# Kernel tuning notes

Hardware: AMD Instinct MI355X
Metric: run time of the kernel (lower is better)

Reference implementation:

```python
import jax, jax.numpy as jnp
import numpy as np

H = 31  # hidden_size == input_size


def setup_inputs() -> dict:
    key = jax.random.key(0)
    ks = jax.random.split(key, 7)
    B, T = 2048, 512
    s = 1.0 / np.sqrt(H)
    return {
        "x": jax.random.normal(ks[0], (B, T, H), dtype=jnp.float32),
        "W_ih": jax.random.uniform(ks[1], (3 * H, H), minval=-s, maxval=s, dtype=jnp.float32),
        "W_hh": jax.random.uniform(ks[2], (3 * H, H), minval=-s, maxval=s, dtype=jnp.float32),
        "b_ih": jax.random.uniform(ks[3], (3 * H,), minval=-s, maxval=s, dtype=jnp.float32),
        "b_hh": jax.random.uniform(ks[4], (3 * H,), minval=-s, maxval=s, dtype=jnp.float32),
        "W_fc": jax.random.uniform(ks[5], (2, H), minval=-s, maxval=s, dtype=jnp.float32),
        "b_fc": jax.random.uniform(ks[6], (2,), minval=-s, maxval=s, dtype=jnp.float32),
    }


def _gru_seq(x, W_ih, W_hh, b_ih, b_hh):
    # x: [B, T, I]. Precompute input-side gates for all timesteps (one big GEMM).
    B = x.shape[0]
    xg = jnp.einsum("bti,gi->btg", x, W_ih) + b_ih          # [B, T, 3H]
    xg = jnp.swapaxes(xg, 0, 1)                              # [T, B, 3H]

    def step(h, xg_t):
        gh = h @ W_hh.T + b_hh                               # [B, 3H]
        ir, iz, inn = jnp.split(xg_t, 3, axis=-1)
        hr, hz, hn = jnp.split(gh, 3, axis=-1)
        r = jax.nn.sigmoid(ir + hr)
        z = jax.nn.sigmoid(iz + hz)
        n = jnp.tanh(inn + r * hn)
        h_new = (1.0 - z) * n + z * h
        return h_new, h_new

    h0 = jnp.zeros((B, H), dtype=x.dtype)
    _, out = jax.lax.scan(step, h0, xg)                      # out: [T, B, H]
    return jnp.swapaxes(out, 0, 1)                           # [B, T, H]


def reference(x, W_ih, W_hh, b_ih, b_hh, W_fc, b_fc):
    out = _gru_seq(x, W_ih, W_hh, b_ih, b_hh)                # [B, T, H]
    return out @ W_fc.T + b_fc                               # [B, T, 2]
```

## Files before the change

### kernel.cpp

```cpp
#include <hip/hip_runtime.h>


constexpr int BB = 2048, TT = 512, HH = 31;
constexpr int RR = 96;
constexpr size_t XG_BYTES = (size_t)BB * RR * TT * 2;
constexpr int WPAIRS = 93 * 16;
constexpr size_t WS_NEEDED = XG_BYTES + (size_t)WPAIRS * 4;
constexpr float LOG2E = 1.4426950408889634f;

#define MEMFENCE asm volatile("" ::: "memory")

typedef _Float16 hf2 __attribute__((ext_vector_type(2)));

__device__ __forceinline__ float dot2(int a, hf2 w, float acc) {
#if __has_builtin(__builtin_amdgcn_fdot2)
    return __builtin_amdgcn_fdot2(__builtin_bit_cast(hf2, a), w, acc, false);
#else
    hf2 x = __builtin_bit_cast(hf2, a);
    return acc + (float)x.x * (float)w.x + (float)x.y * (float)w.y;
#endif
}

__device__ __forceinline__ float fast_exp2(float x) {
#if __has_builtin(__builtin_amdgcn_exp2f)
    return __builtin_amdgcn_exp2f(x);
#else
    return exp2f(x);
#endif
}
__device__ __forceinline__ float fast_rcp(float x) {
#if __has_builtin(__builtin_amdgcn_rcpf)
    return __builtin_amdgcn_rcpf(x);
#else
    return __fdividef(1.f, x);
#endif
}

#if __has_builtin(__builtin_amdgcn_permlane32_swap)
__device__ __forceinline__ float xor32_swap(float v) {
    auto p = __builtin_amdgcn_permlane32_swap(
        __builtin_bit_cast(unsigned, v), __builtin_bit_cast(unsigned, v),
        false, false);
    return __builtin_bit_cast(float, (unsigned)p[0]) +
           __builtin_bit_cast(float, (unsigned)p[1]) - v;
}
#else
__device__ __forceinline__ float xor32_swap(float v) { return __shfl_xor(v, 32); }
#endif

__device__ __forceinline__ void bcast_h(float hv, int hs[16]) {
    const int pk = __builtin_bit_cast(int, __builtin_amdgcn_cvt_pkrtz(hv, hv));
#if __has_builtin(__builtin_amdgcn_update_dpp)
    const int nb = __builtin_amdgcn_update_dpp(0, pk, 0xB1, 0xF, 0xF, true);
#else
    const int nb = __shfl_xor(pk, 1);
#endif
    const int pr = __builtin_amdgcn_perm(nb, pk, 0x05040100);
#pragma unroll
    for (int m = 0; m < 16; ++m)
        hs[m] = __builtin_amdgcn_readlane(pr, 2 * m);
}

__global__ void pack_wih_kernel(const float* __restrict__ W_ih, int* __restrict__ wpk) {
    int q = blockIdx.x * blockDim.x + threadIdx.x;
    if (q >= WPAIRS) return;
    int row = q >> 4, p = q & 15;
    const float s = (row < 62) ? LOG2E : 2.f * LOG2E;
    float lo = W_ih[row * HH + 2 * p] * s;
    float hi = (2 * p + 1 < HH) ? W_ih[row * HH + 2 * p + 1] * s : 0.f;
    hf2 w; w.x = (_Float16)lo; w.y = (_Float16)hi;
    wpk[q] = __builtin_bit_cast(int, w);
}

__global__ __launch_bounds__(128, 2) void xg_gemm_kernel(
    const float* __restrict__ x, const int* __restrict__ wpk,
    const float* __restrict__ b_ih, _Float16* __restrict__ xg)
{
    const int tid = threadIdx.x;
    const int b   = blockIdx.x;
    const int t0  = tid * 4;
    const float* xb = x + ((size_t)b * TT + t0) * HH;

    hf2 xp[4][16];
#pragma unroll
    for (int j = 0; j < 4; ++j)
#pragma unroll
        for (int p = 0; p < 16; ++p) {
            float lo = xb[j * HH + 2 * p];
            float hi = (2 * p + 1 < HH) ? xb[j * HH + 2 * p + 1] : 0.f;
            xp[j][p].x = (_Float16)lo; xp[j][p].y = (_Float16)hi;
        }

    _Float16* xgb = xg + (size_t)b * RR * TT + t0;
    for (int row = 0; row < 93; ++row) {
        const float bi = b_ih[row] * ((row < 62) ? LOG2E : 2.f * LOG2E);
        float a0 = bi, a1 = bi, a2 = bi, a3 = bi;
        const int* wr = wpk + row * 16;
#pragma unroll
        for (int p = 0; p < 16; ++p) {
            const int w = wr[p];
            a0 = dot2(w, xp[0][p], a0);
            a1 = dot2(w, xp[1][p], a1);
            a2 = dot2(w, xp[2][p], a2);
            a3 = dot2(w, xp[3][p], a3);
        }
        hf2 lo2; lo2.x = (_Float16)a0; lo2.y = (_Float16)a1;
        hf2 hi2; hi2.x = (_Float16)a2; hi2.y = (_Float16)a3;
        *reinterpret_cast<int2*>(xgb + (size_t)row * TT) =
            make_int2(__builtin_bit_cast(int, lo2), __builtin_bit_cast(int, hi2));
    }
    for (int row = 93; row < 96; ++row)
        *reinterpret_cast<int2*>(xgb + (size_t)row * TT) = make_int2(0, 0);
}

__global__ __launch_bounds__(256, 2) void gru_rec_kernel(
    const _Float16* __restrict__ xg, const float* __restrict__ W_hh,
    const float* __restrict__ b_hh, const float* __restrict__ W_fc,
    const float* __restrict__ b_fc, float* __restrict__ out)
{
    const int tid = threadIdx.x, wv = tid >> 6, lane = tid & 63;
    const int li = lane & 31, half = lane >> 5;
    const int b  = blockIdx.x * 4 + wv;
    const bool u = (li < HH);

    const float sA = u ? LOG2E : 1.f;
    const float sN = 2.f * LOG2E;
    const float* pA = u ? W_hh + (size_t)(half * HH + li) * HH
                        : W_fc + (size_t)half * HH;
    const float* pN = W_hh + (size_t)(2 * HH + (u ? li : 0)) * HH;
    const float bA0 = (u ? b_hh[half * HH + li] : b_fc[half]) * sA;
    const float bN0 = u ? b_hh[2 * HH + li] * sN : 0.f;

    hf2 wA[16], wN[16];
#pragma unroll
    for (int p = 0; p < 16; ++p) {
        const float alo = pA[2 * p];
        const float ahi = (2 * p + 1 < HH) ? pA[2 * p + 1] : 0.f;
        wA[p].x = (_Float16)(alo * sA); wA[p].y = (_Float16)(ahi * sA);
        const float nlo = u ? pN[2 * p] : 0.f;
        const float nhi = (u && 2 * p + 1 < HH) ? pN[2 * p + 1] : 0.f;
        wN[p].x = (_Float16)(nlo * sN); wN[p].y = (_Float16)(nhi * sN);
    }

    const int rowA = u ? half * HH + li : 93 + half;
    const int rowN = u ? 2 * HH + li : 95;
    const _Float16* gA = xg + ((size_t)b * RR + rowA) * TT;
    const _Float16* gN = xg + ((size_t)b * RR + rowN) * TT;
    float* outb = out + (size_t)b * TT * 2;

    float hval = 0.f;
    int hs[16];
    bcast_h(0.f, hs);

    int4 bufA = *(const int4*)gA;
    int4 bufN = *(const int4*)gN;

    for (int tb = 0; tb < TT / 8; ++tb) {
        int4 nxtA = bufA, nxtN = bufN;
        if (tb + 1 < TT / 8) {
            nxtA = *(const int4*)(gA + (size_t)(tb + 1) * 8);
            nxtN = *(const int4*)(gN + (size_t)(tb + 1) * 8);
        }
#pragma unroll
        for (int s = 0; s < 8; ++s) {
            const int t = tb * 8 + s;
            const float xa = (float)(((const _Float16*)&bufA)[s]);
            const float xn = (float)(((const _Float16*)&bufN)[s]);

            float a0 = bA0 + xa, a1 = 0.f, n0 = bN0, n1 = 0.f;
#pragma unroll
            for (int m = 0; m < 16; m += 2) {
                a0 = dot2(hs[m],     wA[m],     a0);
                a1 = dot2(hs[m + 1], wA[m + 1], a1);
                n0 = dot2(hs[m],     wN[m],     n0);
                n1 = dot2(hs[m + 1], wN[m + 1], n1);
            }
            const float accA = a0 + a1;
            const float accN = n0 + n1;
            const float asw = xor32_swap(accA);

            if (li == 31 && t > 0) outb[(size_t)(t - 1) * 2 + half] = accA;

            const float g  = fast_rcp(1.f + fast_exp2(-accA));
            const float go = fast_rcp(1.f + fast_exp2(-asw));
            const float r = half ? go : g;
            const float z = half ? g : go;
            const float en = fast_exp2(fmaf(-r, accN, -xn));
            const float nn = fmaf(2.f, fast_rcp(1.f + en), -1.f);
            const float hnew = nn + z * (hval - nn);
            hval = u ? hnew : 0.f;
            bcast_h(hval, hs);
        }
        bufA = nxtA; bufN = nxtN;
    }

    {
        float a0 = bA0, a1 = 0.f;
#pragma unroll
        for (int m = 0; m < 16; m += 2) {
            a0 = dot2(hs[m],     wA[m],     a0);
            a1 = dot2(hs[m + 1], wA[m + 1], a1);
        }
        if (li == 31) outb[(size_t)(TT - 1) * 2 + half] = a0 + a1;
    }
}

__global__ __launch_bounds__(64, 1) void gru_pair_kernel(
    const float* __restrict__ x, const float* __restrict__ W_ih,
    const float* __restrict__ W_hh, const float* __restrict__ b_ih,
    const float* __restrict__ b_hh, const float* __restrict__ W_fc,
    const float* __restrict__ b_fc, float* __restrict__ out)
{
    __shared__ _Float16 hbuf[2][32];
    __shared__ _Float16 xbuf[2][2][32];

    const int lane = threadIdx.x & 63;
    const int li   = lane & 31;
    const int half = lane >> 5;
    const int b    = blockIdx.x * 2 + half;
    const bool unit = (li < HH);

    const float* ph0 = unit ? W_hh + (size_t)li * HH            : W_fc;
    const float* ph1 = unit ? W_hh + (size_t)(HH + li) * HH     : W_fc + HH;
    const float* ph2 = unit ? W_hh + (size_t)(2 * HH + li) * HH : nullptr;
    const float* px0 = unit ? W_ih + (size_t)li * HH            : nullptr;
    const float* px1 = unit ? W_ih + (size_t)(HH + li) * HH     : nullptr;
    const float* px2 = unit ? W_ih + (size_t)(2 * HH + li) * HH : nullptr;

    hf2 wh0[16], wh1[16], wh2[16], wx0[16], wx1[16], wx2[16];
#pragma unroll
    for (int m = 0; m < 16; ++m) {
        auto pk = [&](const float* p) -> hf2 {
            hf2 r;
            r.x = p ? (_Float16)p[2 * m] : (_Float16)0.f;
            r.y = (p && (2 * m + 1) < HH) ? (_Float16)p[2 * m + 1] : (_Float16)0.f;
            return r;
        };
        wh0[m] = pk(ph0); wh1[m] = pk(ph1); wh2[m] = pk(ph2);
        wx0[m] = pk(px0); wx1[m] = pk(px1); wx2[m] = pk(px2);
    }

    float arH0, azH0, anH0, anX0;
    if (unit) {
        arH0 = b_ih[li] + b_hh[li];
        azH0 = b_ih[HH + li] + b_hh[HH + li];
        anH0 = b_hh[2 * HH + li];
        anX0 = b_ih[2 * HH + li];
    } else {
        arH0 = b_fc[0]; azH0 = b_fc[1]; anH0 = 0.f; anX0 = 0.f;
    }

    const float* xb   = x + (size_t)b * TT * HH;
    float*       outb = out + (size_t)b * TT * 2;

    hbuf[half][li]    = (_Float16)0.f;
    xbuf[0][half][li] = unit ? (_Float16)xb[li]      : (_Float16)0.f;
    xbuf[1][half][li] = unit ? (_Float16)xb[HH + li] : (_Float16)0.f;
    MEMFENCE;
    float xpre = unit ? xb[(size_t)2 * HH + li] : 0.f;
    float hval = 0.f;

    const int4* HP  = (const int4*)(&hbuf[half][0]);
    const int4* XB0 = (const int4*)(&xbuf[0][half][0]);
    const int4* XB1 = (const int4*)(&xbuf[1][half][0]);

    int4 xq0 = XB0[0], xq1 = XB0[1], xq2 = XB0[2], xq3 = XB0[3];

#pragma unroll 2
    for (int t = 0; t < TT; ++t) {
        int4 hq0 = HP[0], hq1 = HP[1], hq2 = HP[2], hq3 = HP[3];

        float arH = arH0, azH = azH0, anH = anH0;
        float arX = 0.f, azX = 0.f, anX = anX0;
#define STEPM(m, hp, xp) \
        arH = dot2(hp, wh0[m], arH); azH = dot2(hp, wh1[m], azH); \
        anH = dot2(hp, wh2[m], anH); arX = dot2(xp, wx0[m], arX); \
        azX = dot2(xp, wx1[m], azX); anX = dot2(xp, wx2[m], anX);
        STEPM(0,  hq0.x, xq0.x) STEPM(1,  hq0.y, xq0.y)
        STEPM(2,  hq0.z, xq0.z) STEPM(3,  hq0.w, xq0.w)
        STEPM(4,  hq1.x, xq1.x) STEPM(5,  hq1.y, xq1.y)
        STEPM(6,  hq1.z, xq1.z) STEPM(7,  hq1.w, xq1.w)
        STEPM(8,  hq2.x, xq2.x) STEPM(9,  hq2.y, xq2.y)
        STEPM(10, hq2.z, xq2.z) STEPM(11, hq2.w, xq2.w)
        STEPM(12, hq3.x, xq3.x) STEPM(13, hq3.y, xq3.y)
        STEPM(14, hq3.z, xq3.z) STEPM(15, hq3.w, xq3.w)
#undef STEPM

        const float sumr = arH + arX;
        const float sumz = azH + azX;
        if (lane == 31 && t > 0)
            *(float2*)(outb + (size_t)(t - 1) * 2) = make_float2(sumr, sumz);

        const float r    = __fdividef(1.f, 1.f + __expf(-sumr));
        const float z    = __fdividef(1.f, 1.f + __expf(-sumz));
        const float npre = fmaf(r, anH, anX);
        const float nn   = __fdividef(2.f, 1.f + __expf(-2.f * npre)) - 1.f;
        const float hnew = nn + z * (hval - nn);
        hval = unit ? hnew : 0.f;
        hbuf[half][li] = (_Float16)hval;

        xbuf[t & 1][half][li] = unit ? (_Float16)xpre : (_Float16)0.f;
        MEMFENCE;
        int tn = t + 3; if (tn > TT - 1) tn = TT - 1;
        xpre = unit ? xb[(size_t)tn * HH + li] : 0.f;

        const int4* XN = (t & 1) ? XB0 : XB1;
        xq0 = XN[0]; xq1 = XN[1]; xq2 = XN[2]; xq3 = XN[3];
    }

    {
        int4 hq0 = HP[0], hq1 = HP[1], hq2 = HP[2], hq3 = HP[3];
        float f0 = arH0, f1 = azH0;
#define FST(m, hp) f0 = dot2(hp, wh0[m], f0); f1 = dot2(hp, wh1[m], f1);
        FST(0,  hq0.x) FST(1,  hq0.y) FST(2,  hq0.z) FST(3,  hq0.w)
        FST(4,  hq1.x) FST(5,  hq1.y) FST(6,  hq1.z) FST(7,  hq1.w)
        FST(8,  hq2.x) FST(9,  hq2.y) FST(10, hq2.z) FST(11, hq2.w)
        FST(12, hq3.x) FST(13, hq3.y) FST(14, hq3.z) FST(15, hq3.w)
#undef FST
        if (lane == 31)
            *(float2*)(outb + (size_t)(TT - 1) * 2) = make_float2(f0, f1);
    }
}

extern "C" void kernel_launch(void* const* d_in, const int* in_sizes, int n_in,
                              void* d_out, int out_size, void* d_ws, size_t ws_size,
                              hipStream_t stream) {
    const float* x    = (const float*)d_in[0];
    const float* W_ih = (const float*)d_in[1];
    const float* W_hh = (const float*)d_in[2];
    const float* b_ih = (const float*)d_in[3];
    const float* b_hh = (const float*)d_in[4];
    const float* W_fc = (const float*)d_in[5];
    const float* b_fc = (const float*)d_in[6];
    float* out = (float*)d_out;

    if (ws_size >= WS_NEEDED) {
        _Float16* xg = (_Float16*)d_ws;
        int* wpk = (int*)((char*)d_ws + XG_BYTES);
        pack_wih_kernel<<<(WPAIRS + 255) / 256, 256, 0, stream>>>(W_ih, wpk);
        xg_gemm_kernel<<<BB, 128, 0, stream>>>(x, wpk, b_ih, xg);
        gru_rec_kernel<<<BB / 4, 256, 0, stream>>>(xg, W_hh, b_hh, W_fc, b_fc, out);
    } else {
        gru_pair_kernel<<<BB / 2, 64, 0, stream>>>(x, W_ih, W_hh, b_ih, b_hh,
                                                   W_fc, b_fc, out);
    }
}
```

Measured before the change: 299.4 us.

## Split GRU recurrence across two waves per sequence with LDS hidden-state exchange

Each batch row now runs in its own 128-thread block with two waves, each wave owning a subset of the gate rows (r and n in one wave, z plus gate evaluation in the other). Gate pre-activations and the new hidden state pass through shared memory with two block barriers per timestep, replacing the register-resident readlane broadcast and cross-half swap. This halves the per-lane dot-product work and raises the number of resident waves. In exchange it adds two __syncthreads and LDS round-trips to every serial timestep, which lengthens the critical path.

```diff
diff --git a/kernel.cpp b/kernel.cpp
--- a/kernel.cpp
+++ b/kernel.cpp
@@ -34,31 +34,6 @@
 #else
     return __fdividef(1.f, x);
 #endif
-}
-
-#if __has_builtin(__builtin_amdgcn_permlane32_swap)
-__device__ __forceinline__ float xor32_swap(float v) {
-    auto p = __builtin_amdgcn_permlane32_swap(
-        __builtin_bit_cast(unsigned, v), __builtin_bit_cast(unsigned, v),
-        false, false);
-    return __builtin_bit_cast(float, (unsigned)p[0]) +
-           __builtin_bit_cast(float, (unsigned)p[1]) - v;
-}
-#else
-__device__ __forceinline__ float xor32_swap(float v) { return __shfl_xor(v, 32); }
-#endif
-
-__device__ __forceinline__ void bcast_h(float hv, int hs[16]) {
-    const int pk = __builtin_bit_cast(int, __builtin_amdgcn_cvt_pkrtz(hv, hv));
-#if __has_builtin(__builtin_amdgcn_update_dpp)
-    const int nb = __builtin_amdgcn_update_dpp(0, pk, 0xB1, 0xF, 0xF, true);
-#else
-    const int nb = __shfl_xor(pk, 1);
-#endif
-    const int pr = __builtin_amdgcn_perm(nb, pk, 0x05040100);
-#pragma unroll
-    for (int m = 0; m < 16; ++m)
-        hs[m] = __builtin_amdgcn_readlane(pr, 2 * m);
 }
 
 __global__ void pack_wih_kernel(const float* __restrict__ W_ih, int* __restrict__ wpk) {
@@ -113,95 +88,117 @@
         *reinterpret_cast<int2*>(xgb + (size_t)row * TT) = make_int2(0, 0);
 }
 
-__global__ __launch_bounds__(256, 2) void gru_rec_kernel(
+__global__ __launch_bounds__(128, 4) void gru_rec2_kernel(
     const _Float16* __restrict__ xg, const float* __restrict__ W_hh,
     const float* __restrict__ b_hh, const float* __restrict__ W_fc,
     const float* __restrict__ b_fc, float* __restrict__ out)
 {
-    const int tid = threadIdx.x, wv = tid >> 6, lane = tid & 63;
-    const int li = lane & 31, half = lane >> 5;
-    const int b  = blockIdx.x * 4 + wv;
-    const bool u = (li < HH);
-
-    const float sA = u ? LOG2E : 1.f;
-    const float sN = 2.f * LOG2E;
-    const float* pA = u ? W_hh + (size_t)(half * HH + li) * HH
-                        : W_fc + (size_t)half * HH;
-    const float* pN = W_hh + (size_t)(2 * HH + (u ? li : 0)) * HH;
-    const float bA0 = (u ? b_hh[half * HH + li] : b_fc[half]) * sA;
-    const float bN0 = u ? b_hh[2 * HH + li] * sN : 0.f;
-
-    hf2 wA[16], wN[16];
+    __shared__ float2    pre2[128];
+    __shared__ _Float16  hbuf[32];
+
+    const int tid  = threadIdx.x;
+    const int wave = tid >> 6;
+    const int li   = tid & 63;
+    const int b    = blockIdx.x;
+    const int u    = li & 31;
+
+    const bool loRole = (li < 31);
+    const bool hiRole = (li >= 32 && li < 63);
+    const bool isFC   = (li == 63);
+    const bool isN    = (wave == 0) && hiRole;
+    const bool isGate = (wave == 1) && hiRole;
+
+    int   row   = 95;
+    const float* wrow = nullptr;
+    float scale = 0.f, bias = 0.f;
+    int   slot  = 96 + (tid & 31);
+    if (loRole) {
+        row = wave * 31 + u;
+        wrow = W_hh + (size_t)row * HH; scale = LOG2E;
+        bias = LOG2E * b_hh[row];     slot = row;
+    } else if (isN) {
+        row = 62 + u;
+        wrow = W_hh + (size_t)row * HH; scale = 2.f * LOG2E;
+        bias = 2.f * LOG2E * b_hh[row]; slot = row;
+    } else if (isFC) {
+        wrow = W_fc + (size_t)wave * HH; scale = 1.f;
+        bias = b_fc[wave];
+    }
+
+    hf2 wD[16];
 #pragma unroll
     for (int p = 0; p < 16; ++p) {
-        const float alo = pA[2 * p];
-        const float ahi = (2 * p + 1 < HH) ? pA[2 * p + 1] : 0.f;
-        wA[p].x = (_Float16)(alo * sA); wA[p].y = (_Float16)(ahi * sA);
-        const float nlo = u ? pN[2 * p] : 0.f;
-        const float nhi = (u && 2 * p + 1 < HH) ? pN[2 * p + 1] : 0.f;
-        wN[p].x = (_Float16)(nlo * sN); wN[p].y = (_Float16)(nhi * sN);
-    }
-
-    const int rowA = u ? half * HH + li : 93 + half;
-    const int rowN = u ? 2 * HH + li : 95;
-    const _Float16* gA = xg + ((size_t)b * RR + rowA) * TT;
-    const _Float16* gN = xg + ((size_t)b * RR + rowN) * TT;
+        float lo = wrow ? wrow[2 * p] * scale : 0.f;
+        float hi = (wrow && 2 * p + 1 < HH) ? wrow[2 * p + 1] * scale : 0.f;
+        wD[p].x = (_Float16)lo; wD[p].y = (_Float16)hi;
+    }
+
+    const _Float16* gA = xg + ((size_t)b * RR + row) * TT;
     float* outb = out + (size_t)b * TT * 2;
 
-    float hval = 0.f;
-    int hs[16];
-    bcast_h(0.f, hs);
-
+    if (tid < 32) hbuf[tid] = (_Float16)0.f;
+    __syncthreads();
+
+    const int4* HP = (const int4*)&hbuf[0];
+    int4 hq0 = HP[0], hq1 = HP[1], hq2 = HP[2], hq3 = HP[3];
+
+    float hold = 0.f;
     int4 bufA = *(const int4*)gA;
-    int4 bufN = *(const int4*)gN;
 
     for (int tb = 0; tb < TT / 8; ++tb) {
-        int4 nxtA = bufA, nxtN = bufN;
-        if (tb + 1 < TT / 8) {
-            nxtA = *(const int4*)(gA + (size_t)(tb + 1) * 8);
-            nxtN = *(const int4*)(gN + (size_t)(tb + 1) * 8);
-        }
+        int4 nxtA = bufA;
+        if (tb + 1 < TT / 8) nxtA = *(const int4*)(gA + (size_t)(tb + 1) * 8);
 #pragma unroll
         for (int s = 0; s < 8; ++s) {
             const int t = tb * 8 + s;
             const float xa = (float)(((const _Float16*)&bufA)[s]);
-            const float xn = (float)(((const _Float16*)&bufN)[s]);
-
-            float a0 = bA0 + xa, a1 = 0.f, n0 = bN0, n1 = 0.f;
-#pragma unroll
-            for (int m = 0; m < 16; m += 2) {
-                a0 = dot2(hs[m],     wA[m],     a0);
-                a1 = dot2(hs[m + 1], wA[m + 1], a1);
-                n0 = dot2(hs[m],     wN[m],     n0);
-                n1 = dot2(hs[m + 1], wN[m + 1], n1);
+
+            float a0 = bias + (isN ? 0.f : xa), a1 = 0.f;
+            a0 = dot2(hq0.x, wD[0],  a0); a1 = dot2(hq0.y, wD[1],  a1);
+            a0 = dot2(hq0.z, wD[2],  a0); a1 = dot2(hq0.w, wD[3],  a1);
+            a0 = dot2(hq1.x, wD[4],  a0); a1 = dot2(hq1.y, wD[5],  a1);
+            a0 = dot2(hq1.z, wD[6],  a0); a1 = dot2(hq1.w, wD[7],  a1);
+            a0 = dot2(hq2.x, wD[8],  a0); a1 = dot2(hq2.y, wD[9],  a1);
+            a0 = dot2(hq2.z, wD[10], a0); a1 = dot2(hq2.w, wD[11], a1);
+            a0 = dot2(hq3.x, wD[12], a0); a1 = dot2(hq3.y, wD[13], a1);
+            a0 = dot2(hq3.z, wD[14], a0); a1 = dot2(hq3.w, wD[15], a1);
+            const float acc = a0 + a1;
+
+            pre2[slot] = make_float2(acc, xa);
+            if (isFC && t > 0) outb[(size_t)(t - 1) * 2 + wave] = acc;
+
+            __syncthreads();
+
+            if (isGate) {
+                const float  pr = pre2[u].x;
+                const float  pz = pre2[31 + u].x;
+                const float2 pn = pre2[62 + u];
+                const float r  = fast_rcp(1.f + fast_exp2(-pr));
+                const float z  = fast_rcp(1.f + fast_exp2(-pz));
+                const float en = fast_exp2(-fmaf(r, pn.x, pn.y));
+                const float nn = fmaf(2.f, fast_rcp(1.f + en), -1.f);
+                const float h  = nn + z * (hold - nn);
+                hold = h;
+                hbuf[u] = (_Float16)h;
             }
-            const float accA = a0 + a1;
-            const float accN = n0 + n1;
-            const float asw = xor32_swap(accA);
-
-            if (li == 31 && t > 0) outb[(size_t)(t - 1) * 2 + half] = accA;
-
-            const float g  = fast_rcp(1.f + fast_exp2(-accA));
-            const float go = fast_rcp(1.f + fast_exp2(-asw));
-            const float r = half ? go : g;
-            const float z = half ? g : go;
-            const float en = fast_exp2(fmaf(-r, accN, -xn));
-            const float nn = fmaf(2.f, fast_rcp(1.f + en), -1.f);
-            const float hnew = nn + z * (hval - nn);
-            hval = u ? hnew : 0.f;
-            bcast_h(hval, hs);
+            __syncthreads();
+
+            hq0 = HP[0]; hq1 = HP[1]; hq2 = HP[2]; hq3 = HP[3];
         }
-        bufA = nxtA; bufN = nxtN;
+        bufA = nxtA;
     }
 
     {
-        float a0 = bA0, a1 = 0.f;
-#pragma unroll
-        for (int m = 0; m < 16; m += 2) {
-            a0 = dot2(hs[m],     wA[m],     a0);
-            a1 = dot2(hs[m + 1], wA[m + 1], a1);
-        }
-        if (li == 31) outb[(size_t)(TT - 1) * 2 + half] = a0 + a1;
+        float a0 = bias, a1 = 0.f;
+        a0 = dot2(hq0.x, wD[0],  a0); a1 = dot2(hq0.y, wD[1],  a1);
+        a0 = dot2(hq0.z, wD[2],  a0); a1 = dot2(hq0.w, wD[3],  a1);
+        a0 = dot2(hq1.x, wD[4],  a0); a1 = dot2(hq1.y, wD[5],  a1);
+        a0 = dot2(hq1.z, wD[6],  a0); a1 = dot2(hq1.w, wD[7],  a1);
+        a0 = dot2(hq2.x, wD[8],  a0); a1 = dot2(hq2.y, wD[9],  a1);
+        a0 = dot2(hq2.z, wD[10], a0); a1 = dot2(hq2.w, wD[11], a1);
+        a0 = dot2(hq3.x, wD[12], a0); a1 = dot2(hq3.y, wD[13], a1);
+        a0 = dot2(hq3.z, wD[14], a0); a1 = dot2(hq3.w, wD[15], a1);
+        if (isFC) outb[(size_t)(TT - 1) * 2 + wave] = a0 + a1;
     }
 }
 
@@ -339,7 +336,7 @@
         int* wpk = (int*)((char*)d_ws + XG_BYTES);
         pack_wih_kernel<<<(WPAIRS + 255) / 256, 256, 0, stream>>>(W_ih, wpk);
         xg_gemm_kernel<<<BB, 128, 0, stream>>>(x, wpk, b_ih, xg);
-        gru_rec_kernel<<<BB / 4, 256, 0, stream>>>(xg, W_hh, b_hh, W_fc, b_fc, out);
+        gru_rec2_kernel<<<BB, 128, 0, stream>>>(xg, W_hh, b_hh, W_fc, b_fc, out);
     } else {
         gru_pair_kernel<<<BB / 2, 64, 0, stream>>>(x, W_ih, W_hh, b_ih, b_hh,
                                                    W_fc, b_fc, out);
```

Measured after the change: 333.7 us. 1.11x slower.

## Compute GRU recurrent matvec with MFMA and LDS-broadcast hidden state

Applied to the files above, without the earlier changes.

Replaces the per-lane packed-fp16 dot-product recurrence (two sequences per wavefront with readlane broadcast) with one sequence per wavefront. Each step computes the 96-row W_hh/W_fc matvec via six 16x16x32 fp16 MFMAs whose B operand is the hidden state read from LDS. Gate preactivations are exchanged through shared memory and the gate math runs on 31 lanes. This uses matrix cores, but most of each MFMA output is redundant and every step now adds LDS round trips on the serial critical path.

```diff
diff --git a/kernel.cpp b/kernel.cpp
--- a/kernel.cpp
+++ b/kernel.cpp
@@ -11,6 +11,8 @@
 #define MEMFENCE asm volatile("" ::: "memory")
 
 typedef _Float16 hf2 __attribute__((ext_vector_type(2)));
+typedef _Float16 hf8 __attribute__((ext_vector_type(8)));
+typedef float f32x4 __attribute__((ext_vector_type(4)));
 
 __device__ __forceinline__ float dot2(int a, hf2 w, float acc) {
 #if __has_builtin(__builtin_amdgcn_fdot2)
@@ -34,31 +36,6 @@
 #else
     return __fdividef(1.f, x);
 #endif
-}
-
-#if __has_builtin(__builtin_amdgcn_permlane32_swap)
-__device__ __forceinline__ float xor32_swap(float v) {
-    auto p = __builtin_amdgcn_permlane32_swap(
-        __builtin_bit_cast(unsigned, v), __builtin_bit_cast(unsigned, v),
-        false, false);
-    return __builtin_bit_cast(float, (unsigned)p[0]) +
-           __builtin_bit_cast(float, (unsigned)p[1]) - v;
-}
-#else
-__device__ __forceinline__ float xor32_swap(float v) { return __shfl_xor(v, 32); }
-#endif
-
-__device__ __forceinline__ void bcast_h(float hv, int hs[16]) {
-    const int pk = __builtin_bit_cast(int, __builtin_amdgcn_cvt_pkrtz(hv, hv));
-#if __has_builtin(__builtin_amdgcn_update_dpp)
-    const int nb = __builtin_amdgcn_update_dpp(0, pk, 0xB1, 0xF, 0xF, true);
-#else
-    const int nb = __shfl_xor(pk, 1);
-#endif
-    const int pr = __builtin_amdgcn_perm(nb, pk, 0x05040100);
-#pragma unroll
-    for (int m = 0; m < 16; ++m)
-        hs[m] = __builtin_amdgcn_readlane(pr, 2 * m);
 }
 
 __global__ void pack_wih_kernel(const float* __restrict__ W_ih, int* __restrict__ wpk) {
@@ -113,95 +90,123 @@
         *reinterpret_cast<int2*>(xgb + (size_t)row * TT) = make_int2(0, 0);
 }
 
-__global__ __launch_bounds__(256, 2) void gru_rec_kernel(
+__global__ __launch_bounds__(64, 2) void gru_mfma_kernel(
     const _Float16* __restrict__ xg, const float* __restrict__ W_hh,
     const float* __restrict__ b_hh, const float* __restrict__ W_fc,
     const float* __restrict__ b_fc, float* __restrict__ out)
 {
-    const int tid = threadIdx.x, wv = tid >> 6, lane = tid & 63;
-    const int li = lane & 31, half = lane >> 5;
-    const int b  = blockIdx.x * 4 + wv;
-    const bool u = (li < HH);
-
-    const float sA = u ? LOG2E : 1.f;
-    const float sN = 2.f * LOG2E;
-    const float* pA = u ? W_hh + (size_t)(half * HH + li) * HH
-                        : W_fc + (size_t)half * HH;
-    const float* pN = W_hh + (size_t)(2 * HH + (u ? li : 0)) * HH;
-    const float bA0 = (u ? b_hh[half * HH + li] : b_fc[half]) * sA;
-    const float bN0 = u ? b_hh[2 * HH + li] * sN : 0.f;
-
-    hf2 wA[16], wN[16];
-#pragma unroll
-    for (int p = 0; p < 16; ++p) {
-        const float alo = pA[2 * p];
-        const float ahi = (2 * p + 1 < HH) ? pA[2 * p + 1] : 0.f;
-        wA[p].x = (_Float16)(alo * sA); wA[p].y = (_Float16)(ahi * sA);
-        const float nlo = u ? pN[2 * p] : 0.f;
-        const float nhi = (u && 2 * p + 1 < HH) ? pN[2 * p + 1] : 0.f;
-        wN[p].x = (_Float16)(nlo * sN); wN[p].y = (_Float16)(nhi * sN);
-    }
-
-    const int rowA = u ? half * HH + li : 93 + half;
-    const int rowN = u ? 2 * HH + li : 95;
-    const _Float16* gA = xg + ((size_t)b * RR + rowA) * TT;
-    const _Float16* gN = xg + ((size_t)b * RR + rowN) * TT;
+    __shared__ float    preF[96];
+    __shared__ _Float16 hbuf[32];
+
+    const int lane = threadIdx.x & 63;
+    const int col  = lane & 15;
+    const int grp  = lane >> 4;
+    const int b    = blockIdx.x;
+
+    hf8 A[6];
+#pragma unroll
+    for (int c = 0; c < 6; ++c) {
+        const int row = 16 * c + col;
+#pragma unroll
+        for (int e = 0; e < 8; ++e) {
+            const int k = grp * 8 + e;
+            float v = 0.f;
+            if (k < HH) {
+                if (row < 62)       v = LOG2E * W_hh[row * HH + k];
+                else if (row < 93)  v = 2.f * LOG2E * W_hh[row * HH + k];
+                else if (row >= 94) v = W_fc[(row - 94) * HH + k];
+            }
+            A[c][e] = (_Float16)v;
+        }
+    }
+    f32x4 CB[6];
+#pragma unroll
+    for (int c = 0; c < 6; ++c)
+#pragma unroll
+        for (int j = 0; j < 4; ++j) {
+            const int row = 16 * c + 4 * grp + j;
+            float v;
+            if (row < 62)       v = LOG2E * b_hh[row];
+            else if (row < 93)  v = 2.f * LOG2E * b_hh[row];
+            else if (row == 93) v = 0.f;
+            else                v = b_fc[row - 94];
+            CB[c][j] = v;
+        }
+
+    int rR = 93, rZ = 93, rN = 93;
+    if (lane < HH) { rR = lane; rZ = HH + lane; rN = 2 * HH + lane; }
+    const _Float16* gR = xg + ((size_t)b * RR + rR) * TT;
+    const _Float16* gZ = xg + ((size_t)b * RR + rZ) * TT;
+    const _Float16* gN = xg + ((size_t)b * RR + rN) * TT;
     float* outb = out + (size_t)b * TT * 2;
 
-    float hval = 0.f;
-    int hs[16];
-    bcast_h(0.f, hs);
-
-    int4 bufA = *(const int4*)gA;
-    int4 bufN = *(const int4*)gN;
+    if (lane < 32) hbuf[lane] = (_Float16)0.f;
+    MEMFENCE;
+
+    float hold = 0.f;
+    int4 bR = *(const int4*)gR;
+    int4 bZ = *(const int4*)gZ;
+    int4 bN = *(const int4*)gN;
+
+    const char* hb_base = (const char*)&hbuf[0] + (grp << 4);
 
     for (int tb = 0; tb < TT / 8; ++tb) {
-        int4 nxtA = bufA, nxtN = bufN;
+        int4 nR = bR, nZ = bZ, nN = bN;
         if (tb + 1 < TT / 8) {
-            nxtA = *(const int4*)(gA + (size_t)(tb + 1) * 8);
-            nxtN = *(const int4*)(gN + (size_t)(tb + 1) * 8);
+            nR = *(const int4*)(gR + (size_t)(tb + 1) * 8);
+            nZ = *(const int4*)(gZ + (size_t)(tb + 1) * 8);
+            nN = *(const int4*)(gN + (size_t)(tb + 1) * 8);
         }
 #pragma unroll
         for (int s = 0; s < 8; ++s) {
             const int t = tb * 8 + s;
-            const float xa = (float)(((const _Float16*)&bufA)[s]);
-            const float xn = (float)(((const _Float16*)&bufN)[s]);
-
-            float a0 = bA0 + xa, a1 = 0.f, n0 = bN0, n1 = 0.f;
-#pragma unroll
-            for (int m = 0; m < 16; m += 2) {
-                a0 = dot2(hs[m],     wA[m],     a0);
-                a1 = dot2(hs[m + 1], wA[m + 1], a1);
-                n0 = dot2(hs[m],     wN[m],     n0);
-                n1 = dot2(hs[m + 1], wN[m + 1], n1);
+            const hf8 Bf = __builtin_bit_cast(hf8, *(const int4*)hb_base);
+            const f32x4 D0 = __builtin_amdgcn_mfma_f32_16x16x32_f16(A[0], Bf, CB[0], 0, 0, 0);
+            const f32x4 D1 = __builtin_amdgcn_mfma_f32_16x16x32_f16(A[1], Bf, CB[1], 0, 0, 0);
+            const f32x4 D2 = __builtin_amdgcn_mfma_f32_16x16x32_f16(A[2], Bf, CB[2], 0, 0, 0);
+            const f32x4 D3 = __builtin_amdgcn_mfma_f32_16x16x32_f16(A[3], Bf, CB[3], 0, 0, 0);
+            const f32x4 D4 = __builtin_amdgcn_mfma_f32_16x16x32_f16(A[4], Bf, CB[4], 0, 0, 0);
+            const f32x4 D5 = __builtin_amdgcn_mfma_f32_16x16x32_f16(A[5], Bf, CB[5], 0, 0, 0);
+            MEMFENCE;
+            if (col == 0) {
+                *(f32x4*)&preF[ 0 + 4 * grp] = D0;
+                *(f32x4*)&preF[16 + 4 * grp] = D1;
+                *(f32x4*)&preF[32 + 4 * grp] = D2;
+                *(f32x4*)&preF[48 + 4 * grp] = D3;
+                *(f32x4*)&preF[64 + 4 * grp] = D4;
+                *(f32x4*)&preF[80 + 4 * grp] = D5;
             }
-            const float accA = a0 + a1;
-            const float accN = n0 + n1;
-            const float asw = xor32_swap(accA);
-
-            if (li == 31 && t > 0) outb[(size_t)(t - 1) * 2 + half] = accA;
-
-            const float g  = fast_rcp(1.f + fast_exp2(-accA));
-            const float go = fast_rcp(1.f + fast_exp2(-asw));
-            const float r = half ? go : g;
-            const float z = half ? g : go;
-            const float en = fast_exp2(fmaf(-r, accN, -xn));
-            const float nn = fmaf(2.f, fast_rcp(1.f + en), -1.f);
-            const float hnew = nn + z * (hval - nn);
-            hval = u ? hnew : 0.f;
-            bcast_h(hval, hs);
-        }
-        bufA = nxtA; bufN = nxtN;
+            MEMFENCE;
+            if (lane < HH) {
+                const float xar = (float)(((const _Float16*)&bR)[s]);
+                const float xaz = (float)(((const _Float16*)&bZ)[s]);
+                const float xn  = (float)(((const _Float16*)&bN)[s]);
+                const float pr  = preF[lane]          + xar;
+                const float pz  = preF[HH + lane]     + xaz;
+                const float pn  = preF[2 * HH + lane];
+                const float r   = fast_rcp(1.f + fast_exp2(-pr));
+                const float z   = fast_rcp(1.f + fast_exp2(-pz));
+                const float en  = fast_exp2(-fmaf(r, pn, xn));
+                const float nn  = fmaf(2.f, fast_rcp(1.f + en), -1.f);
+                hold = nn + z * (hold - nn);
+                hbuf[lane] = (_Float16)hold;
+            } else if (lane == HH && t > 0) {
+                const float2 fc = *(const float2*)&preF[94];
+                *(float2*)(outb + (size_t)(t - 1) * 2) = fc;
+            }
+            MEMFENCE;
+        }
+        bR = nR; bZ = nZ; bN = nN;
     }
 
     {
-        float a0 = bA0, a1 = 0.f;
-#pragma unroll
-        for (int m = 0; m < 16; m += 2) {
-            a0 = dot2(hs[m],     wA[m],     a0);
-            a1 = dot2(hs[m + 1], wA[m + 1], a1);
-        }
-        if (li == 31) outb[(size_t)(TT - 1) * 2 + half] = a0 + a1;
+        const hf8 Bf = __builtin_bit_cast(hf8, *(const int4*)hb_base);
+        const f32x4 D5 = __builtin_amdgcn_mfma_f32_16x16x32_f16(A[5], Bf, CB[5], 0, 0, 0);
+        MEMFENCE;
+        if (col == 0) *(f32x4*)&preF[80 + 4 * grp] = D5;
+        MEMFENCE;
+        if (lane == HH)
+            *(float2*)(outb + (size_t)(TT - 1) * 2) = *(const float2*)&preF[94];
     }
 }
 
@@ -339,7 +344,7 @@
         int* wpk = (int*)((char*)d_ws + XG_BYTES);
         pack_wih_kernel<<<(WPAIRS + 255) / 256, 256, 0, stream>>>(W_ih, wpk);
         xg_gemm_kernel<<<BB, 128, 0, stream>>>(x, wpk, b_ih, xg);
-        gru_rec_kernel<<<BB / 4, 256, 0, stream>>>(xg, W_hh, b_hh, W_fc, b_fc, out);
+        gru_mfma_kernel<<<BB, 64, 0, stream>>>(xg, W_hh, b_hh, W_fc, b_fc, out);
     } else {
         gru_pair_kernel<<<BB / 2, 64, 0, stream>>>(x, W_ih, W_hh, b_ih, b_hh,
                                                    W_fc, b_fc, out);
```

New measurement: 404.3 us. +35.0%, slower.
